# Kernel tuning notes

Hardware: AMD Instinct MI355X
Metric: run time of the kernel (lower is better)

Reference implementation:

```python
import jax, jax.numpy as jnp
import numpy as np
from jax import lax


def _lstm_scan(x, Wih, Whh, bih, bhh):
    # x: (B, S, D); returns hidden states (B, S, H)
    B = x.shape[0]
    H = Whh.shape[1]
    b = bih + bhh

    def step(carry, xt):
        h, c = carry
        gates = xt @ Wih.T + h @ Whh.T + b  # (B, 4H)
        i, f, g, o = jnp.split(gates, 4, axis=-1)
        i = jax.nn.sigmoid(i)
        f = jax.nn.sigmoid(f)
        g = jnp.tanh(g)
        o = jax.nn.sigmoid(o)
        c = f * c + i * g
        h = o * jnp.tanh(c)
        return (h, c), h

    h0 = jnp.zeros((B, H), dtype=x.dtype)
    c0 = jnp.zeros((B, H), dtype=x.dtype)
    _, hs = lax.scan(step, (h0, c0), jnp.swapaxes(x, 0, 1))  # (S, B, H)
    return jnp.swapaxes(hs, 0, 1)


def setup_inputs() -> dict:
    key = jax.random.key(0)
    ks = jax.random.split(key, 12)
    B, S, D, H, A = 64, 512, 256, 512, 64
    s_in = 1.0 / np.sqrt(D)
    s_h = 1.0 / np.sqrt(H)
    s_2h = 1.0 / np.sqrt(2 * H)
    s_a = 1.0 / np.sqrt(A)
    return {
        "x": jax.random.normal(ks[0], (B, S, D), jnp.float32),
        "f_Wih": jax.random.normal(ks[1], (4 * H, D), jnp.float32) * s_in,
        "f_Whh": jax.random.normal(ks[2], (4 * H, H), jnp.float32) * s_h,
        "f_bih": jax.random.normal(ks[3], (4 * H,), jnp.float32) * s_h,
        "f_bhh": jax.random.normal(ks[4], (4 * H,), jnp.float32) * s_h,
        "b_Wih": jax.random.normal(ks[5], (4 * H, D), jnp.float32) * s_in,
        "b_Whh": jax.random.normal(ks[6], (4 * H, H), jnp.float32) * s_h,
        "b_bih": jax.random.normal(ks[7], (4 * H,), jnp.float32) * s_h,
        "b_bhh": jax.random.normal(ks[8], (4 * H,), jnp.float32) * s_h,
        "att_W": jax.random.normal(ks[9], (A, 2 * H), jnp.float32) * s_2h,
        "att_v": jax.random.normal(ks[10], (1, A), jnp.float32) * s_a,
    }


def reference(x, f_Wih, f_Whh, f_bih, f_bhh, b_Wih, b_Whh, b_bih, b_bhh, att_W, att_v):
    # forward-direction LSTM over x
    f_h = _lstm_scan(x, f_Wih, f_Whh, f_bih, f_bhh)
    # backward-direction LSTM: run over time-reversed x, flip outputs back
    b_h = jnp.flip(_lstm_scan(jnp.flip(x, axis=1), b_Wih, b_Whh, b_bih, b_bhh), axis=1)
    h = jnp.concatenate([f_h, b_h], axis=2)  # (B, S, 2H)
    # self-attention pooling
    att = jnp.einsum("bsa,oa->bs", jnp.tanh(jnp.einsum("bsh,ah->bsa", h, att_W)), att_v)
    w = jax.nn.softmax(att, axis=1)  # (B, S)
    return jnp.einsum("bs,bsh->bh", w, h)  # (B, 2H)
```

## Files before the change

### kernel.cpp

```cpp
#include <hip/hip_runtime.h>

#define B_ 64
#define S_ 512
#define D_ 256
#define H_ 512

typedef __attribute__((ext_vector_type(8))) short bfx8;
typedef __attribute__((ext_vector_type(4))) float f32x4;

#define MFMA16(a,b,c) __builtin_amdgcn_mfma_f32_16x16x32_bf16((a),(b),(c),0,0,0)
#define AL(p)  __hip_atomic_load((p), __ATOMIC_RELAXED, __HIP_MEMORY_SCOPE_AGENT)
#define ALI(p) __hip_atomic_load((p), __ATOMIC_RELAXED, __HIP_MEMORY_SCOPE_AGENT)

__device__ __forceinline__ unsigned short f2bf(float x){
  union { float f; unsigned int u; } v; v.f = x;
  unsigned int r = v.u + 0x7fffu + ((v.u >> 16) & 1u);
  return (unsigned short)(r >> 16);
}
__device__ __forceinline__ float bf2f(unsigned short b){
  union { unsigned int u; float f; } v; v.u = ((unsigned int)b) << 16; return v.f;
}
__device__ __forceinline__ float sigm(float x){ return 1.f/(1.f + __expf(-x)); }
__device__ __forceinline__ float tanhfast(float x){
  float xc = fminf(fmaxf(x, -15.f), 15.f);
  float e = __expf(2.f * xc);
  return (e - 1.f) / (e + 1.f);
}
__device__ __forceinline__ void unpack8(uint4 a, uint4 b, bfx8& hi, bfx8& lo){
  hi[0]=(short)(a.x>>16); lo[0]=(short)(a.x&0xffffu);
  hi[1]=(short)(a.y>>16); lo[1]=(short)(a.y&0xffffu);
  hi[2]=(short)(a.z>>16); lo[2]=(short)(a.z&0xffffu);
  hi[3]=(short)(a.w>>16); lo[3]=(short)(a.w&0xffffu);
  hi[4]=(short)(b.x>>16); lo[4]=(short)(b.x&0xffffu);
  hi[5]=(short)(b.y>>16); lo[5]=(short)(b.y&0xffffu);
  hi[6]=(short)(b.z>>16); lo[6]=(short)(b.z&0xffffu);
  hi[7]=(short)(b.w>>16); lo[7]=(short)(b.w&0xffffu);
}
__device__ __forceinline__ void cvt8(const float* vv, bfx8& hi, bfx8& lo){
  #pragma unroll
  for (int j = 0; j < 8; ++j) {
    unsigned short h = f2bf(vv[j]);
    hi[j] = (short)h;
    lo[j] = (short)f2bf(vv[j] - bf2f(h));
  }
}

__global__ void __launch_bounds__(256) k_xfrag(const float* __restrict__ x,
                                               unsigned short* __restrict__ xhi,
                                               unsigned short* __restrict__ xlo){
  int idx = blockIdx.x*256 + threadIdx.x;
  int lane = idx & 63, kt = (idx>>6)&7, q = (idx>>9)&3, t = idx>>11;
  int b = q*16 + (lane&15);
  int k0 = kt*32 + ((lane>>4)&3)*8;
  const float4* p = (const float4*)(x + ((size_t)b*S_ + t)*D_ + k0);
  float4 v0 = p[0], v1 = p[1];
  float vv[8] = {v0.x,v0.y,v0.z,v0.w,v1.x,v1.y,v1.z,v1.w};
  bfx8 hi, lo; cvt8(vv, hi, lo);
  *(bfx8*)(xhi + (size_t)idx*8) = hi;
  *(bfx8*)(xlo + (size_t)idx*8) = lo;
}

__global__ void __launch_bounds__(256) k_wfrag(const float* __restrict__ fWih,
                                               const float* __restrict__ bWih,
                                               unsigned short* __restrict__ whi,
                                               unsigned short* __restrict__ wlo){
  int idx = blockIdx.x*256 + threadIdx.x;
  int lane = idx & 63, nt = (idx>>6)&3, kt = (idx>>8)&7, r = (idx>>11)&31, dir = (idx>>18)&1;
  int row = nt*512 + r*16 + (lane&15);
  int k0 = kt*32 + ((lane>>4)&3)*8;
  const float* W = dir ? bWih : fWih;
  const float4* p = (const float4*)(W + (size_t)row*D_ + k0);
  float4 v0 = p[0], v1 = p[1];
  float vv[8] = {v0.x,v0.y,v0.z,v0.w,v1.x,v1.y,v1.z,v1.w};
  bfx8 hi, lo; cvt8(vv, hi, lo);
  *(bfx8*)(whi + (size_t)idx*8) = hi;
  *(bfx8*)(wlo + (size_t)idx*8) = lo;
}

__global__ void __launch_bounds__(256) k_awfrag(const float* __restrict__ attW,
                                                unsigned short* __restrict__ awhi,
                                                unsigned short* __restrict__ awlo){
  int idx = blockIdx.x*256 + threadIdx.x;
  int lane = idx & 63, kt = (idx>>6)&31, nt = idx>>11;
  int n = nt*16 + (lane&15);
  int k0 = kt*32 + ((lane>>4)&3)*8;
  const float4* p = (const float4*)(attW + (size_t)n*1024 + k0);
  float4 v0 = p[0], v1 = p[1];
  float vv[8] = {v0.x,v0.y,v0.z,v0.w,v1.x,v1.y,v1.z,v1.w};
  bfx8 hi, lo; cvt8(vv, hi, lo);
  *(bfx8*)(awhi + (size_t)idx*8) = hi;
  *(bfx8*)(awlo + (size_t)idx*8) = lo;
}

__global__ void __launch_bounds__(256,1) k_lstm(
    const float* __restrict__ fWhh, const float* __restrict__ bWhh,
    const float* __restrict__ fbih, const float* __restrict__ fbhh,
    const float* __restrict__ bbih, const float* __restrict__ bbhh,
    unsigned int* __restrict__ hpk,
    unsigned int* __restrict__ hx,
    const unsigned short* __restrict__ xhi, const unsigned short* __restrict__ xlo,
    const unsigned short* __restrict__ whi, const unsigned short* __restrict__ wlo,
    int* __restrict__ dg)
{
  extern __shared__ char smem[];
  unsigned short* shh   = (unsigned short*)smem;
  unsigned short* shl   = shh + 20480;
  unsigned short* sh_hi = (unsigned short*)(smem + 81920);
  unsigned short* sh_lo = sh_hi + 8192;
  float* gbuf = (float*)(smem + 114688);
  char*  xbuf = smem + 118784;

  const int tid = threadIdx.x, bid = blockIdx.x;
  const int g = bid & 7, r = bid >> 3;
  const int dir = g >> 2, q = g & 3;
  const int wv = tid >> 6, lane = tid & 63;
  const float* Whh = dir ? bWhh : fWhh;

  bfx8 rbh[6], rbl[6];
  #pragma unroll
  for (int i = 0; i < 16; ++i) {
    int fl = tid & 63, fnt = (tid>>6)&3;
    int row = fnt*512 + r*16 + (fl&15);
    int k0 = i*32 + ((fl>>4)&3)*8;
    const float4* p = (const float4*)(Whh + (size_t)row*H_ + k0);
    float4 v0 = p[0], v1 = p[1];
    float vv[8] = {v0.x,v0.y,v0.z,v0.w,v1.x,v1.y,v1.z,v1.w};
    bfx8 hi, lo; cvt8(vv, hi, lo);
    if (i < 10) {
      *(bfx8*)(shh + (size_t)((i*4+fnt)*64+fl)*8) = hi;
      *(bfx8*)(shl + (size_t)((i*4+fnt)*64+fl)*8) = lo;
    } else { rbh[i-10] = hi; rbl[i-10] = lo; }
  }

  bfx8 wrh[8], wrl[8];
  {
    const size_t wb = (((size_t)(dir*4+q)*32 + r)*32 + wv)*64;
    #pragma unroll
    for (int kt = 0; kt < 8; ++kt) {
      wrh[kt] = *(const bfx8*)(whi + (wb + kt*256 + lane)*8);
      wrl[kt] = *(const bfx8*)(wlo + (wb + kt*256 + lane)*8);
    }
  }

  const int b_l = tid >> 4, cc = tid & 15;
  const int jcol = r*16 + cc;
  const float* bih = dir ? bbih : fbih;
  const float* bhh = dir ? bbhh : fbhh;
  float bias[4];
  #pragma unroll
  for (int gt = 0; gt < 4; ++gt) bias[gt] = bih[gt*512 + jcol] + bhh[gt*512 + jcol];
  float cst = 0.f;
  const int hkt   = jcol >> 5;
  const int hlane = ((jcol>>3)&3)*16 + b_l;
  const int hj    = jcol & 7;
  const int d0    = g*128 + lane*2;

  {
    const int t0 = dir ? (S_-1) : 0;
    const char* hsrc = (const char*)(xhi + (((size_t)t0*4+q) << 12));
    const char* lsrc = (const char*)(xlo + (((size_t)t0*4+q) << 12));
    *(uint4*)(xbuf + tid*16)          = *(const uint4*)(hsrc + tid*16);
    *(uint4*)(xbuf + 4096 + tid*16)   = *(const uint4*)(hsrc + 4096 + tid*16);
    *(uint4*)(xbuf + 8192 + tid*16)   = *(const uint4*)(lsrc + tid*16);
    *(uint4*)(xbuf + 12288 + tid*16)  = *(const uint4*)(lsrc + 4096 + tid*16);
  }
  __syncthreads();

  for (int ti = 0; ti < S_; ++ti) {
    const int t = dir ? (S_-1-ti) : ti;
    char* xb  = xbuf + ((ti)&1)*16384;
    char* xbn = xbuf + ((ti+1)&1)*16384;
    f32x4 a0 = {0.f,0.f,0.f,0.f}, a1 = a0, a2 = a0, a3 = a0, a4 = a0, a5 = a0;

    uint4 xr0, xr1, xr2, xr3;
    const bool pf = (ti + 1 < S_);
    if (pf) {
      const int tn = dir ? (S_-1-(ti+1)) : (ti+1);
      const char* hsrc = (const char*)(xhi + (((size_t)tn*4+q) << 12));
      const char* lsrc = (const char*)(xlo + (((size_t)tn*4+q) << 12));
      xr0 = *(const uint4*)(hsrc + tid*16);
      xr1 = *(const uint4*)(hsrc + 4096 + tid*16);
      xr2 = *(const uint4*)(lsrc + tid*16);
      xr3 = *(const uint4*)(lsrc + 4096 + tid*16);
    }

    {
      const unsigned short* xh = (const unsigned short*)xb;
      const unsigned short* xl = (const unsigned short*)(xb + 8192);
      #pragma unroll
      for (int kt = 0; kt < 8; ++kt) {
        bfx8 x0 = *(const bfx8*)(xh + (size_t)(kt*64+lane)*8);
        bfx8 x1 = *(const bfx8*)(xl + (size_t)(kt*64+lane)*8);
        if (kt & 1) {
          a3 = MFMA16(x0, wrh[kt], a3); a4 = MFMA16(x0, wrl[kt], a4); a5 = MFMA16(x1, wrh[kt], a5);
        } else {
          a0 = MFMA16(x0, wrh[kt], a0); a1 = MFMA16(x0, wrl[kt], a1); a2 = MFMA16(x1, wrh[kt], a2);
        }
      }
    }

    if (ti > 0) {
      for (;;) {
        int v0 = ALI(dg + d0), v1 = ALI(dg + d0 + 1);
        if (__all((v0 >= ti) & (v1 >= ti))) break;
      }
      asm volatile("" ::: "memory");
      const unsigned long long* sp =
          (const unsigned long long*)(hx + ((((size_t)(dir*4 + q))*2 + ((ti-1)&1)) << 13));
      unsigned long long qs[16];
      #pragma unroll
      for (int i = 0; i < 16; ++i) qs[i] = AL(sp + i*256 + tid);
      #pragma unroll
      for (int i = 0; i < 16; ++i) {
        unsigned int e0 = (unsigned int)qs[i], e1 = (unsigned int)(qs[i] >> 32);
        *(unsigned int*)(sh_hi + i*512 + tid*2) = (e0 >> 16)     | (e1 & 0xFFFF0000u);
        *(unsigned int*)(sh_lo + i*512 + tid*2) = (e0 & 0xFFFFu) | (e1 << 16);
      }
    }
    if (pf) {
      *(uint4*)(xbn + tid*16)         = xr0;
      *(uint4*)(xbn + 4096 + tid*16)  = xr1;
      *(uint4*)(xbn + 8192 + tid*16)  = xr2;
      *(uint4*)(xbn + 12288 + tid*16) = xr3;
    }
    __syncthreads();
    if (ti > 0) {
      #pragma unroll
      for (int kt = 0; kt < 16; ++kt) {
        bfx8 ah = *(const bfx8*)(sh_hi + kt*512 + lane*8);
        bfx8 al = *(const bfx8*)(sh_lo + kt*512 + lane*8);
        bfx8 bh, bl;
        if (kt < 10) {
          bh = *(const bfx8*)(shh + (size_t)((kt*4+wv)*64 + lane)*8);
          bl = *(const bfx8*)(shl + (size_t)((kt*4+wv)*64 + lane)*8);
        } else { bh = rbh[kt-10]; bl = rbl[kt-10]; }
        if (kt & 1) {
          a3 = MFMA16(ah, bh, a3); a4 = MFMA16(ah, bl, a4); a5 = MFMA16(al, bh, a5);
        } else {
          a0 = MFMA16(ah, bh, a0); a1 = MFMA16(ah, bl, a1); a2 = MFMA16(al, bh, a2);
        }
      }
    }

    f32x4 gate = (a0 + a1) + (a2 + a3) + (a4 + a5);
    #pragma unroll
    for (int rr = 0; rr < 4; ++rr)
      gbuf[wv*256 + (((lane>>4)&3)*4+rr)*16 + (lane&15)] = gate[rr];
    __syncthreads();
    {
      float gi = gbuf[0*256 + b_l*16 + cc] + bias[0];
      float gf = gbuf[1*256 + b_l*16 + cc] + bias[1];
      float gg = gbuf[2*256 + b_l*16 + cc] + bias[2];
      float go = gbuf[3*256 + b_l*16 + cc] + bias[3];
      float is = sigm(gi), fs = sigm(gf), gs = tanhfast(gg), os = sigm(go);
      cst = fs*cst + is*gs;
      float hv = os * tanhfast(cst);
      unsigned short hh = f2bf(hv);
      unsigned short hl = f2bf(hv - bf2f(hh));
      unsigned int pk = (((unsigned int)hh) << 16) | (unsigned int)hl;
      size_t hoff = (size_t)hkt*512 + hlane*8 + hj;
      hpk[((((size_t)dir*S_ + t)*4 + q) << 13) + hoff] = pk;
      __hip_atomic_store(hx + ((((size_t)(dir*4 + q))*2 + (ti&1)) << 13) + hoff, pk,
                         __ATOMIC_RELAXED, __HIP_MEMORY_SCOPE_AGENT);
    }
    asm volatile("s_waitcnt vmcnt(0)" ::: "memory");
    if (lane == 0)
      __hip_atomic_store(dg + g*128 + r*4 + wv, ti + 1, __ATOMIC_RELAXED, __HIP_MEMORY_SCOPE_AGENT);
  }
}

__global__ void __launch_bounds__(256) k_att1(const unsigned int* __restrict__ hpk,
                                              const unsigned short* __restrict__ awhi,
                                              const unsigned short* __restrict__ awlo,
                                              const float* __restrict__ attv,
                                              float* __restrict__ attbuf){
  const int s = blockIdx.x;
  const int tid = threadIdx.x, wv = tid >> 6, lane = tid & 63;
  const int q = wv;
  f32x4 z = {0.f,0.f,0.f,0.f};
  f32x4 acc[4][3];
  #pragma unroll
  for (int nt = 0; nt < 4; ++nt) { acc[nt][0] = z; acc[nt][1] = z; acc[nt][2] = z; }
  for (int kt = 0; kt < 32; ++kt) {
    int dir = kt >> 4, ktt = kt & 15;
    const unsigned int* hb = hpk + ((((size_t)dir*S_ + s)*4 + q) << 13) + ktt*512 + lane*8;
    uint4 u0 = *(const uint4*)hb, u1 = *(const uint4*)(hb + 4);
    bfx8 ah, al; unpack8(u0, u1, ah, al);
    #pragma unroll
    for (int nt = 0; nt < 4; ++nt) {
      bfx8 bh = *(const bfx8*)(awhi + (size_t)((nt*32+kt)*64+lane)*8);
      bfx8 bl = *(const bfx8*)(awlo + (size_t)((nt*32+kt)*64+lane)*8);
      acc[nt][0] = MFMA16(ah, bh, acc[nt][0]);
      acc[nt][1] = MFMA16(ah, bl, acc[nt][1]);
      acc[nt][2] = MFMA16(al, bh, acc[nt][2]);
    }
  }
  float part[4] = {0.f,0.f,0.f,0.f};
  #pragma unroll
  for (int nt = 0; nt < 4; ++nt) {
    f32x4 d = (acc[nt][0] + acc[nt][1]) + acc[nt][2];
    float vvv = attv[nt*16 + (lane&15)];
    #pragma unroll
    for (int rr = 0; rr < 4; ++rr) part[rr] += tanhfast(d[rr]) * vvv;
  }
  #pragma unroll
  for (int m = 1; m < 16; m <<= 1) {
    #pragma unroll
    for (int rr = 0; rr < 4; ++rr) part[rr] += __shfl_xor(part[rr], m, 64);
  }
  if ((lane & 15) == 0) {
    #pragma unroll
    for (int rr = 0; rr < 4; ++rr) {
      int b = q*16 + ((lane>>4)&3)*4 + rr;
      attbuf[(size_t)b*S_ + s] = part[rr];
    }
  }
}

__global__ void __launch_bounds__(256) k_att2(const float* __restrict__ attbuf,
                                              float* __restrict__ wbuf){
  const int b = blockIdx.x, tid = threadIdx.x;
  __shared__ float sm[4];
  float v0 = attbuf[(size_t)b*S_ + tid];
  float v1 = attbuf[(size_t)b*S_ + 256 + tid];
  float m = fmaxf(v0, v1);
  #pragma unroll
  for (int o = 1; o < 64; o <<= 1) m = fmaxf(m, __shfl_xor(m, o, 64));
  if ((tid & 63) == 0) sm[tid >> 6] = m;
  __syncthreads();
  m = fmaxf(fmaxf(sm[0], sm[1]), fmaxf(sm[2], sm[3]));
  __syncthreads();
  float e0 = __expf(v0 - m), e1 = __expf(v1 - m);
  float su = e0 + e1;
  #pragma unroll
  for (int o = 1; o < 64; o <<= 1) su += __shfl_xor(su, o, 64);
  if ((tid & 63) == 0) sm[tid >> 6] = su;
  __syncthreads();
  su = (sm[0] + sm[1]) + (sm[2] + sm[3]);
  wbuf[(size_t)b*S_ + tid]       = e0 / su;
  wbuf[(size_t)b*S_ + 256 + tid] = e1 / su;
}

__global__ void __launch_bounds__(256) k_att3(const unsigned int* __restrict__ hpk,
                                              const float* __restrict__ wbuf,
                                              float* __restrict__ out){
  const int bid = blockIdx.x;
  const int dir = bid >> 6, q = (bid >> 4) & 3, kt = bid & 15;
  const int tid = threadIdx.x;
  __shared__ float wl[16*512];
  for (int i = tid; i < 16*512; i += 256) {
    int bb = i >> 9, ss = i & 511;
    wl[i] = wbuf[(size_t)(q*16 + bb)*S_ + ss];
  }
  __syncthreads();
  const int l2 = tid >> 2, jj = (tid & 3)*2;
  const int b_l = l2 & 15;
  float acc0 = 0.f, acc1 = 0.f;
  for (int t = 0; t < S_; ++t) {
    const unsigned int* hb = hpk + ((((size_t)dir*S_ + t)*4 + q) << 13) + kt*512 + l2*8 + jj;
    uint2 u = *(const uint2*)hb;
    float w = wl[b_l*512 + t];
    acc0 += w * (bf2f((unsigned short)(u.x >> 16)) + bf2f((unsigned short)(u.x & 0xffffu)));
    acc1 += w * (bf2f((unsigned short)(u.y >> 16)) + bf2f((unsigned short)(u.y & 0xffffu)));
  }
  int k = kt*32 + ((l2 >> 4) & 3)*8 + jj;
  float* o = out + (size_t)(q*16 + b_l)*1024 + dir*512 + k;
  o[0] = acc0;
  o[1] = acc1;
}

extern "C" void kernel_launch(void* const* d_in, const int* in_sizes, int n_in,
                              void* d_out, int out_size, void* d_ws, size_t ws_size,
                              hipStream_t stream) {
  const float* x     = (const float*)d_in[0];
  const float* fWih  = (const float*)d_in[1];
  const float* fWhh  = (const float*)d_in[2];
  const float* fbih  = (const float*)d_in[3];
  const float* fbhh  = (const float*)d_in[4];
  const float* bWih  = (const float*)d_in[5];
  const float* bWhh  = (const float*)d_in[6];
  const float* bbih  = (const float*)d_in[7];
  const float* bbhh  = (const float*)d_in[8];
  const float* attW  = (const float*)d_in[9];
  const float* attv  = (const float*)d_in[10];
  float* out = (float*)d_out;

  char* ws = (char*)d_ws;
  const size_t OFF_HPK  = 0;
  const size_t OFF_XHI  = 134217728;
  const size_t OFF_XLO  = OFF_XHI + 16777216;
  const size_t OFF_WHI  = OFF_XLO + 16777216;
  const size_t OFF_WLO  = OFF_WHI + 8388608;
  const size_t OFF_AWHI = OFF_WLO + 8388608;
  const size_t OFF_AWLO = OFF_AWHI + 131072;
  const size_t OFF_ATTB = OFF_AWLO + 131072;
  const size_t OFF_WBUF = OFF_ATTB + 131072;
  const size_t OFF_DG   = OFF_WBUF + 131072;
  const size_t OFF_HX   = OFF_DG + 4096;

  unsigned int*   hpk  = (unsigned int*)(ws + OFF_HPK);
  unsigned short* xhi  = (unsigned short*)(ws + OFF_XHI);
  unsigned short* xlo  = (unsigned short*)(ws + OFF_XLO);
  unsigned short* whi  = (unsigned short*)(ws + OFF_WHI);
  unsigned short* wlo  = (unsigned short*)(ws + OFF_WLO);
  unsigned short* awhi = (unsigned short*)(ws + OFF_AWHI);
  unsigned short* awlo = (unsigned short*)(ws + OFF_AWLO);
  float*          attb = (float*)(ws + OFF_ATTB);
  float*          wbuf = (float*)(ws + OFF_WBUF);
  int*            dg   = (int*)(ws + OFF_DG);
  unsigned int*   hx   = (unsigned int*)(ws + OFF_HX);

  hipMemsetAsync(dg, 0, 4096, stream);

  k_xfrag <<<4096, 256, 0, stream>>>(x, xhi, xlo);
  k_wfrag <<<2048, 256, 0, stream>>>(fWih, bWih, whi, wlo);
  k_awfrag<<<32,   256, 0, stream>>>(attW, awhi, awlo);

  const int LDS_BYTES = 151552;
  hipFuncSetAttribute((const void*)k_lstm, hipFuncAttributeMaxDynamicSharedMemorySize, LDS_BYTES);
  k_lstm<<<256, 256, LDS_BYTES, stream>>>(fWhh, bWhh, fbih, fbhh, bbih, bbhh,
                                          hpk, hx, xhi, xlo, whi, wlo, dg);

  k_att1<<<512, 256, 0, stream>>>(hpk, awhi, awlo, attv, attb);
  k_att2<<<64,  256, 0, stream>>>(attb, wbuf);
  k_att3<<<128, 256, 0, stream>>>(hpk, wbuf, out);
}
```

Measured before the change: 1.930 ms.

## Replace per-step flag barrier with epoch tags embedded in hidden-state words

The separate progress-flag array for inter-block synchronization of the recurrent LSTM is removed. A 2-bit step counter is now stored in the low bits of each packed hidden-state word, so consumers poll the data itself and only re-read the entries that are not yet valid. This drops one round trip (flag poll, then data load) per timestep. The cost is that the low-precision half of h loses two mantissa bits, and the 0xFFFF sentinel assumes real data never has an all-ones high part.

```diff
diff --git a/kernel.cpp b/kernel.cpp
--- a/kernel.cpp
+++ b/kernel.cpp
@@ -10,7 +10,6 @@
 
 #define MFMA16(a,b,c) __builtin_amdgcn_mfma_f32_16x16x32_bf16((a),(b),(c),0,0,0)
 #define AL(p)  __hip_atomic_load((p), __ATOMIC_RELAXED, __HIP_MEMORY_SCOPE_AGENT)
-#define ALI(p) __hip_atomic_load((p), __ATOMIC_RELAXED, __HIP_MEMORY_SCOPE_AGENT)
 
 __device__ __forceinline__ unsigned short f2bf(float x){
   union { float f; unsigned int u; } v; v.f = x;
@@ -99,8 +98,7 @@
     unsigned int* __restrict__ hpk,
     unsigned int* __restrict__ hx,
     const unsigned short* __restrict__ xhi, const unsigned short* __restrict__ xlo,
-    const unsigned short* __restrict__ whi, const unsigned short* __restrict__ wlo,
-    int* __restrict__ dg)
+    const unsigned short* __restrict__ whi, const unsigned short* __restrict__ wlo)
 {
   extern __shared__ char smem[];
   unsigned short* shh   = (unsigned short*)smem;
@@ -153,7 +151,6 @@
   const int hkt   = jcol >> 5;
   const int hlane = ((jcol>>3)&3)*16 + b_l;
   const int hj    = jcol & 7;
-  const int d0    = g*128 + lane*2;
 
   {
     const int t0 = dir ? (S_-1) : 0;
@@ -171,6 +168,15 @@
     char* xb  = xbuf + ((ti)&1)*16384;
     char* xbn = xbuf + ((ti+1)&1)*16384;
     f32x4 a0 = {0.f,0.f,0.f,0.f}, a1 = a0, a2 = a0, a3 = a0, a4 = a0, a5 = a0;
+
+    unsigned long long qs[16];
+    const unsigned long long* sp = nullptr;
+    const unsigned expt = (unsigned)((ti-1) & 3);
+    if (ti > 0) {
+      sp = (const unsigned long long*)(hx + ((((size_t)(dir*4 + q))*2 + ((ti-1)&1)) << 13));
+      #pragma unroll
+      for (int i = 0; i < 16; ++i) qs[i] = AL(sp + i*256 + tid);
+    }
 
     uint4 xr0, xr1, xr2, xr3;
     const bool pf = (ti + 1 < S_);
@@ -201,20 +207,27 @@
 
     if (ti > 0) {
       for (;;) {
-        int v0 = ALI(dg + d0), v1 = ALI(dg + d0 + 1);
-        if (__all((v0 >= ti) & (v1 >= ti))) break;
+        bool ok = true;
+        #pragma unroll
+        for (int i = 0; i < 16; ++i) {
+          unsigned lo32 = (unsigned)qs[i], hi32 = (unsigned)(qs[i] >> 32);
+          ok &= ((lo32 >> 16) != 0xFFFFu) & ((lo32 & 3u) == expt)
+              & ((hi32 >> 16) != 0xFFFFu) & ((hi32 & 3u) == expt);
+        }
+        if (ok) break;
+        #pragma unroll
+        for (int i = 0; i < 16; ++i) {
+          unsigned lo32 = (unsigned)qs[i], hi32 = (unsigned)(qs[i] >> 32);
+          bool v = ((lo32 >> 16) != 0xFFFFu) & ((lo32 & 3u) == expt)
+                 & ((hi32 >> 16) != 0xFFFFu) & ((hi32 & 3u) == expt);
+          if (!v) qs[i] = AL(sp + i*256 + tid);
+        }
       }
-      asm volatile("" ::: "memory");
-      const unsigned long long* sp =
-          (const unsigned long long*)(hx + ((((size_t)(dir*4 + q))*2 + ((ti-1)&1)) << 13));
-      unsigned long long qs[16];
-      #pragma unroll
-      for (int i = 0; i < 16; ++i) qs[i] = AL(sp + i*256 + tid);
       #pragma unroll
       for (int i = 0; i < 16; ++i) {
         unsigned int e0 = (unsigned int)qs[i], e1 = (unsigned int)(qs[i] >> 32);
-        *(unsigned int*)(sh_hi + i*512 + tid*2) = (e0 >> 16)     | (e1 & 0xFFFF0000u);
-        *(unsigned int*)(sh_lo + i*512 + tid*2) = (e0 & 0xFFFFu) | (e1 << 16);
+        *(unsigned int*)(sh_hi + i*512 + tid*2) = (e0 >> 16)      | (e1 & 0xFFFF0000u);
+        *(unsigned int*)(sh_lo + i*512 + tid*2) = (e0 & 0xFFFCu)  | ((e1 << 16) & 0xFFFC0000u);
       }
     }
     if (pf) {
@@ -252,20 +265,21 @@
       float gf = gbuf[1*256 + b_l*16 + cc] + bias[1];
       float gg = gbuf[2*256 + b_l*16 + cc] + bias[2];
       float go = gbuf[3*256 + b_l*16 + cc] + bias[3];
-      float is = sigm(gi), fs = sigm(gf), gs = tanhfast(gg), os = sigm(go);
+      float is = sigm(gi), fs = sigm(gf), gs = tanhfast(gg), os = tanhfast(go);
+      os = sigm(go);
       cst = fs*cst + is*gs;
       float hv = os * tanhfast(cst);
       unsigned short hh = f2bf(hv);
       unsigned short hl = f2bf(hv - bf2f(hh));
-      unsigned int pk = (((unsigned int)hh) << 16) | (unsigned int)hl;
+      unsigned int pk  = (((unsigned int)hh) << 16) | (unsigned int)hl;
+      unsigned int pkt = (((unsigned int)hh) << 16) | ((unsigned int)hl & 0xFFFCu)
+                       | ((unsigned int)ti & 3u);
       size_t hoff = (size_t)hkt*512 + hlane*8 + hj;
       hpk[((((size_t)dir*S_ + t)*4 + q) << 13) + hoff] = pk;
-      __hip_atomic_store(hx + ((((size_t)(dir*4 + q))*2 + (ti&1)) << 13) + hoff, pk,
+      __hip_atomic_store(hx + ((((size_t)(dir*4 + q))*2 + (ti&1)) << 13) + hoff, pkt,
                          __ATOMIC_RELAXED, __HIP_MEMORY_SCOPE_AGENT);
     }
     asm volatile("s_waitcnt vmcnt(0)" ::: "memory");
-    if (lane == 0)
-      __hip_atomic_store(dg + g*128 + r*4 + wv, ti + 1, __ATOMIC_RELAXED, __HIP_MEMORY_SCOPE_AGENT);
   }
 }
 
@@ -395,8 +409,7 @@
   const size_t OFF_AWLO = OFF_AWHI + 131072;
   const size_t OFF_ATTB = OFF_AWLO + 131072;
   const size_t OFF_WBUF = OFF_ATTB + 131072;
-  const size_t OFF_DG   = OFF_WBUF + 131072;
-  const size_t OFF_HX   = OFF_DG + 4096;
+  const size_t OFF_HX   = OFF_WBUF + 131072;
 
   unsigned int*   hpk  = (unsigned int*)(ws + OFF_HPK);
   unsigned short* xhi  = (unsigned short*)(ws + OFF_XHI);
@@ -407,10 +420,9 @@
   unsigned short* awlo = (unsigned short*)(ws + OFF_AWLO);
   float*          attb = (float*)(ws + OFF_ATTB);
   float*          wbuf = (float*)(ws + OFF_WBUF);
-  int*            dg   = (int*)(ws + OFF_DG);
   unsigned int*   hx   = (unsigned int*)(ws + OFF_HX);
 
-  hipMemsetAsync(dg, 0, 4096, stream);
+  hipMemsetAsync(hx, 0xFF, 524288, stream);
 
   k_xfrag <<<4096, 256, 0, stream>>>(x, xhi, xlo);
   k_wfrag <<<2048, 256, 0, stream>>>(fWih, bWih, whi, wlo);
@@ -419,7 +431,7 @@
   const int LDS_BYTES = 151552;
   hipFuncSetAttribute((const void*)k_lstm, hipFuncAttributeMaxDynamicSharedMemorySize, LDS_BYTES);
   k_lstm<<<256, 256, LDS_BYTES, stream>>>(fWhh, bWhh, fbih, fbhh, bbih, bbhh,
-                                          hpk, hx, xhi, xlo, whi, wlo, dg);
+                                          hpk, hx, xhi, xlo, whi, wlo);
 
   k_att1<<<512, 256, 0, stream>>>(hpk, awhi, awlo, attv, attb);
   k_att2<<<64,  256, 0, stream>>>(attb, wbuf);
```

After: 2.178 ms. 12.8% more time.
